# Optimization experiments

Measured on AMD Instinct MI355X. Metric: run time of the kernel, lower is better.

Reference implementation:

```python
import jax, jax.numpy as jnp
import numpy as np

N_NODES = 50000
N_EDGES = 800000
N_FEAT = 256
HIDDEN = 64
N_CLASSES = 16
T_END = 3.0  # opt['time']; rk4 takes one step over [0, 3]


def spline_conv(x, src, dst, p, W, R, b, n):
    """SplineConv, dim=1, kernel_size=2, degree=1 open B-spline, aggr='mean'.
    x: [n, Cin]; src/dst: [E]; p: [E,1] pseudo-coords in [0,1];
    W: [2, Cin, Cout]; R: [Cin, Cout]; b: [Cout]."""
    xj = x[src]  # gather source node features [E, Cin]
    # basis weights for K=2, degree=1: (1-p) on kernel 0, p on kernel 1
    msg = ((1.0 - p) * xj) @ W[0] + (p * xj) @ W[1]  # [E, Cout]
    agg = jax.ops.segment_sum(msg, dst, num_segments=n)
    deg = jax.ops.segment_sum(jnp.ones((msg.shape[0], 1), msg.dtype), dst, num_segments=n)
    return agg / jnp.maximum(deg, 1.0) + x @ R + b


def setup_inputs() -> dict:
    key = jax.random.key(0)
    ks = jax.random.split(key, 20)
    x = jax.random.normal(ks[0], (N_NODES, N_FEAT), jnp.float32)
    edge_attr = jax.random.uniform(ks[1], (N_EDGES, 1), jnp.float32)
    src = jax.random.randint(ks[2], (N_EDGES,), 0, N_NODES)
    dst = jax.random.randint(ks[3], (N_EDGES,), 0, N_NODES)

    def w(k, shape, fan_in):
        s = 1.0 / np.sqrt(fan_in)
        return jax.random.uniform(k, shape, jnp.float32, -s, s)

    # conv1: num_features -> hidden
    W1 = w(ks[4], (2, N_FEAT, HIDDEN), N_FEAT)
    R1 = w(ks[5], (N_FEAT, HIDDEN), N_FEAT)
    b1 = jnp.zeros((HIDDEN,), jnp.float32)
    # ODE func: two stacked SplineConvs hidden -> hidden
    Wa = w(ks[6], (2, HIDDEN, HIDDEN), HIDDEN)
    Ra = w(ks[7], (HIDDEN, HIDDEN), HIDDEN)
    ba = jnp.zeros((HIDDEN,), jnp.float32)
    Wb = w(ks[8], (2, HIDDEN, HIDDEN), HIDDEN)
    Rb = w(ks[9], (HIDDEN, HIDDEN), HIDDEN)
    bb = jnp.zeros((HIDDEN,), jnp.float32)
    # conv2: hidden -> num_classes
    W2 = w(ks[10], (2, HIDDEN, N_CLASSES), HIDDEN)
    R2 = w(ks[11], (HIDDEN, N_CLASSES), HIDDEN)
    b2 = jnp.zeros((N_CLASSES,), jnp.float32)

    return dict(x=x, edge_attr=edge_attr, src=src, dst=dst,
                W1=W1, R1=R1, b1=b1, Wa=Wa, Ra=Ra, ba=ba,
                Wb=Wb, Rb=Rb, bb=bb, W2=W2, R2=R2, b2=b2)


def reference(x, edge_attr, src, dst, W1, R1, b1, Wa, Ra, ba, Wb, Rb, bb, W2, R2, b2):
    n = x.shape[0]
    p = edge_attr
    h = jnp.tanh(spline_conv(x, src, dst, p, W1, R1, b1, n))
    # dropout is identity in eval mode

    def f(y):  # GCNLayer: two stacked SplineConvs, no activation
        y = spline_conv(y, src, dst, p, Wa, Ra, ba, n)
        return spline_conv(y, src, dst, p, Wb, Rb, bb, n)

    # single RK4 step from t=0 to t=T_END (torchdiffeq fixed-grid rk4 on s_span=[0,3])
    k1 = f(h)
    k2 = f(h + 0.5 * T_END * k1)
    k3 = f(h + 0.5 * T_END * k2)
    k4 = f(h + T_END * k3)
    h = h + (T_END / 6.0) * (k1 + 2.0 * k2 + 2.0 * k3 + k4)

    out = jnp.tanh(spline_conv(h, src, dst, p, W2, R2, b2, n))
    return jax.nn.log_softmax(out, axis=1)
```

## Files before the change

### kernel.cpp

```cpp
#include <hip/hip_runtime.h>
#include <math.h>

static inline int ceil_div(int a, int b) { return (a + b - 1) / b; }


__global__ __launch_bounds__(256) void zero2(int* __restrict__ a, int* __restrict__ b,
                                             int n) {
    int i = blockIdx.x * 256 + threadIdx.x;
    if (i < n) { a[i] = 0; b[i] = 0; }
}

__global__ __launch_bounds__(256) void hist_kernel(const int* __restrict__ dst,
                                                   int* __restrict__ deg, int E) {
    int e = blockIdx.x * 256 + threadIdx.x;
    if (e < E) atomicAdd(&deg[dst[e]], 1);
}

__global__ __launch_bounds__(256) void scan_blocksum(const int* __restrict__ deg,
                                                     int* __restrict__ bsum, int n) {
    __shared__ int red[256];
    int t = threadIdx.x;
    int base = blockIdx.x * 2048 + t * 8;
    int s = 0;
    #pragma unroll
    for (int i = 0; i < 8; ++i) {
        int idx = base + i;
        if (idx < n) s += deg[idx];
    }
    red[t] = s;
    __syncthreads();
    #pragma unroll
    for (int off = 128; off >= 1; off >>= 1) {
        if (t < off) red[t] += red[t + off];
        __syncthreads();
    }
    if (t == 0) bsum[blockIdx.x] = red[0];
}

__global__ __launch_bounds__(256) void scan_tops(int* __restrict__ bsum, int nb) {
    __shared__ int sh[256];
    int t = threadIdx.x;
    int orig = (t < nb) ? bsum[t] : 0;
    sh[t] = orig;
    __syncthreads();
    for (int off = 1; off < 256; off <<= 1) {
        int add = (t >= off) ? sh[t - off] : 0;
        __syncthreads();
        sh[t] += add;
        __syncthreads();
    }
    if (t < nb) bsum[t] = sh[t] - orig;
}

__global__ __launch_bounds__(256) void scan_final(const int* __restrict__ deg,
                                                  const int* __restrict__ bsum,
                                                  int* __restrict__ rowp,
                                                  float* __restrict__ invd,
                                                  int n, int E) {
    __shared__ int sh[256];
    int t = threadIdx.x;
    int base = blockIdx.x * 2048 + t * 8;
    int loc[8];
    int s = 0;
    #pragma unroll
    for (int i = 0; i < 8; ++i) {
        int idx = base + i;
        int d = (idx < n) ? deg[idx] : 0;
        loc[i] = d;
        s += d;
    }
    sh[t] = s;
    __syncthreads();
    for (int off = 1; off < 256; off <<= 1) {
        int add = (t >= off) ? sh[t - off] : 0;
        __syncthreads();
        sh[t] += add;
        __syncthreads();
    }
    int run = bsum[blockIdx.x] + (sh[t] - s);
    #pragma unroll
    for (int i = 0; i < 8; ++i) {
        int idx = base + i;
        if (idx < n) {
            rowp[idx] = run;
            int d = loc[i];
            run += d;
            invd[idx] = 1.0f / (float)(d > 1 ? d : 1);
        }
    }
    if (blockIdx.x == 0 && t == 0) rowp[n] = E;
}

__global__ __launch_bounds__(256) void scatter_idx(const int* __restrict__ dst,
                                                   const int* __restrict__ rowp,
                                                   int* __restrict__ fill,
                                                   int* __restrict__ ei, int E) {
    int e = blockIdx.x * 256 + threadIdx.x;
    if (e >= E) return;
    int d = dst[e];
    int pos = rowp[d] + atomicAdd(&fill[d], 1);
    ei[pos] = e;
}

__global__ __launch_bounds__(256) void sort_fill(const int* __restrict__ rowp,
                                                 int* __restrict__ ei,
                                                 const int* __restrict__ src,
                                                 const float* __restrict__ p,
                                                 int* __restrict__ es,
                                                 float* __restrict__ ep, int n) {
    int node = blockIdx.x * 256 + threadIdx.x;
    if (node >= n) return;
    int b = rowp[node], e = rowp[node + 1];
    for (int i = b + 1; i < e; ++i) {
        int key = ei[i];
        int j = i - 1;
        while (j >= b && ei[j] > key) { ei[j + 1] = ei[j]; --j; }
        ei[j + 1] = key;
    }
    for (int i = b; i < e; ++i) {
        int id = ei[i];
        es[i] = src[id];
        ep[i] = p[id];
    }
}

__global__ __launch_bounds__(256) void pack_all(
    const float* __restrict__ W1, const float* __restrict__ R1,
    const float* __restrict__ Wa, const float* __restrict__ Ra,
    const float* __restrict__ Wb, const float* __restrict__ Rb,
    const float* __restrict__ W2, const float* __restrict__ R2,
    float* __restrict__ Bc1, float* __restrict__ Bca,
    float* __restrict__ Bcb, float* __restrict__ Bc2) {
    int idx = blockIdx.x * 256 + threadIdx.x;
    const int S1 = 256 * 192, S2 = 192 * 64, S4 = 64 * 48;
    if (idx < S1) {
        int k = idx / 192, c = idx % 192;
        float v;
        if (c < 64)       v = W1[k * 64 + c];
        else if (c < 128) v = W1[256 * 64 + k * 64 + (c - 64)];
        else              v = R1[k * 64 + (c - 128)];
        Bc1[idx] = v;
        return;
    }
    idx -= S1;
    if (idx < S2) { Bca[idx] = (idx < 8192) ? Wa[idx] : Ra[idx - 8192]; return; }
    idx -= S2;
    if (idx < S2) { Bcb[idx] = (idx < 8192) ? Wb[idx] : Rb[idx - 8192]; return; }
    idx -= S2;
    if (idx < S4) {
        int k = idx / 48, c = idx % 48;
        float v;
        if (c < 16)      v = W2[k * 16 + c];
        else if (c < 32) v = W2[64 * 16 + k * 16 + (c - 16)];
        else             v = R2[k * 16 + (c - 32)];
        Bc2[idx] = v;
    }
}

__global__ __launch_bounds__(256) void edge_agg64_v4(const float* __restrict__ x,
                                                     const int* __restrict__ rowp,
                                                     const int* __restrict__ es,
                                                     const float* __restrict__ ep,
                                                     const float* __restrict__ invd,
                                                     float* __restrict__ agg, int n) {
    int gid = blockIdx.x * 256 + threadIdx.x;
    int node = gid >> 4;
    if (node >= n) return;
    int c4 = (gid & 15) << 2;
    int e = rowp[node], eend = rowp[node + 1];
    float sx = 0.f, sy = 0.f, sz = 0.f, sw = 0.f;
    float px = 0.f, py = 0.f, pz = 0.f, pw = 0.f;
    for (; e + 4 <= eend; e += 4) {
        int s0 = es[e], s1 = es[e + 1], s2 = es[e + 2], s3 = es[e + 3];
        float p0 = ep[e], p1 = ep[e + 1], p2 = ep[e + 2], p3 = ep[e + 3];
        float4 v0 = *reinterpret_cast<const float4*>(&x[(size_t)s0 * 64 + c4]);
        float4 v1 = *reinterpret_cast<const float4*>(&x[(size_t)s1 * 64 + c4]);
        float4 v2 = *reinterpret_cast<const float4*>(&x[(size_t)s2 * 64 + c4]);
        float4 v3 = *reinterpret_cast<const float4*>(&x[(size_t)s3 * 64 + c4]);
        sx += (v0.x + v1.x) + (v2.x + v3.x);
        sy += (v0.y + v1.y) + (v2.y + v3.y);
        sz += (v0.z + v1.z) + (v2.z + v3.z);
        sw += (v0.w + v1.w) + (v2.w + v3.w);
        px = fmaf(p0, v0.x, fmaf(p1, v1.x, fmaf(p2, v2.x, fmaf(p3, v3.x, px))));
        py = fmaf(p0, v0.y, fmaf(p1, v1.y, fmaf(p2, v2.y, fmaf(p3, v3.y, py))));
        pz = fmaf(p0, v0.z, fmaf(p1, v1.z, fmaf(p2, v2.z, fmaf(p3, v3.z, pz))));
        pw = fmaf(p0, v0.w, fmaf(p1, v1.w, fmaf(p2, v2.w, fmaf(p3, v3.w, pw))));
    }
    for (; e < eend; ++e) {
        int s = es[e];
        float pe = ep[e];
        float4 v = *reinterpret_cast<const float4*>(&x[(size_t)s * 64 + c4]);
        sx += v.x; sy += v.y; sz += v.z; sw += v.w;
        px = fmaf(pe, v.x, px); py = fmaf(pe, v.y, py);
        pz = fmaf(pe, v.z, pz); pw = fmaf(pe, v.w, pw);
    }
    float w = invd[node];
    float4 a0 = make_float4((sx - px) * w, (sy - py) * w, (sz - pz) * w, (sw - pw) * w);
    float4 a1 = make_float4(px * w, py * w, pz * w, pw * w);
    *reinterpret_cast<float4*>(&agg[(size_t)node * 128 + c4]) = a0;
    *reinterpret_cast<float4*>(&agg[(size_t)node * 128 + 64 + c4]) = a1;
}

__global__ __launch_bounds__(256) void hidden_gemm_db(
    const float* __restrict__ agg, const float* __restrict__ in,
    const float* __restrict__ B, const float* __restrict__ bias,
    int n, int mode, float* __restrict__ u_out,
    const float* __restrict__ hbuf, const float* __restrict__ acc_in,
    float* __restrict__ acc_out, float* __restrict__ t_out,
    float c1, float c2, float c3) {
    __shared__ __align__(16) float As[2][16][68];
    __shared__ __align__(16) float Bs[2][16][68];
    const int t = threadIdx.x;
    const int row0 = blockIdx.x * 64;
    const int ty = t >> 4, tx = t & 15;
    const int lrow = t >> 2, lk = (t & 3) << 2;
    const int bkk = t >> 4, bcol = (t & 15) << 2;

    float4 av = make_float4(0.f, 0.f, 0.f, 0.f);
    {
        int r = row0 + lrow;
        if (r < n) av = *reinterpret_cast<const float4*>(&agg[(size_t)r * 128 + lk]);
    }
    float4 bv = *reinterpret_cast<const float4*>(&B[(size_t)bkk * 64 + bcol]);
    As[0][lk + 0][lrow] = av.x; As[0][lk + 1][lrow] = av.y;
    As[0][lk + 2][lrow] = av.z; As[0][lk + 3][lrow] = av.w;
    *reinterpret_cast<float4*>(&Bs[0][bkk][bcol]) = bv;
    __syncthreads();

    float acc[4][4];
    #pragma unroll
    for (int i = 0; i < 4; ++i)
        #pragma unroll
        for (int j = 0; j < 4; ++j) acc[i][j] = 0.f;

    for (int kt = 0; kt < 12; ++kt) {
        const int cur = kt & 1;
        if (kt + 1 < 12) {
            int k0 = (kt + 1) << 4;
            int r = row0 + lrow;
            int kk = k0 + lk;
            av = make_float4(0.f, 0.f, 0.f, 0.f);
            if (r < n)
                av = (kk < 128)
                    ? *reinterpret_cast<const float4*>(&agg[(size_t)r * 128 + kk])
                    : *reinterpret_cast<const float4*>(&in[(size_t)r * 64 + (kk - 128)]);
            bv = *reinterpret_cast<const float4*>(&B[(size_t)(k0 + bkk) * 64 + bcol]);
        }
        #pragma unroll
        for (int kk = 0; kk < 16; ++kk) {
            float4 a4 = *reinterpret_cast<const float4*>(&As[cur][kk][ty << 2]);
            float4 b4 = *reinterpret_cast<const float4*>(&Bs[cur][kk][tx << 2]);
            float aa[4] = {a4.x, a4.y, a4.z, a4.w};
            float bb[4] = {b4.x, b4.y, b4.z, b4.w};
            #pragma unroll
            for (int i = 0; i < 4; ++i)
                #pragma unroll
                for (int j = 0; j < 4; ++j)
                    acc[i][j] = fmaf(aa[i], bb[j], acc[i][j]);
        }
        if (kt + 1 < 12) {
            const int nx = cur ^ 1;
            As[nx][lk + 0][lrow] = av.x; As[nx][lk + 1][lrow] = av.y;
            As[nx][lk + 2][lrow] = av.z; As[nx][lk + 3][lrow] = av.w;
            *reinterpret_cast<float4*>(&Bs[nx][bkk][bcol]) = bv;
        }
        __syncthreads();
    }

    float4 bia = *reinterpret_cast<const float4*>(&bias[tx << 2]);
    #pragma unroll
    for (int i = 0; i < 4; ++i) {
        int r = row0 + (ty << 2) + i;
        if (r >= n) continue;
        size_t idx = (size_t)r * 64 + (tx << 2);
        float4 v = make_float4(acc[i][0] + bia.x, acc[i][1] + bia.y,
                               acc[i][2] + bia.z, acc[i][3] + bia.w);
        if (mode == 0) {
            *reinterpret_cast<float4*>(&u_out[idx]) = v;
        } else {
            float4 ai = make_float4(0.f, 0.f, 0.f, 0.f);
            if (acc_in) ai = *reinterpret_cast<const float4*>(&acc_in[idx]);
            float4 an = make_float4(ai.x + c3 * v.x, ai.y + c3 * v.y,
                                    ai.z + c3 * v.z, ai.w + c3 * v.w);
            *reinterpret_cast<float4*>(&acc_out[idx]) = an;
            float4 hb = *reinterpret_cast<const float4*>(&hbuf[idx]);
            float4 to = make_float4(hb.x + c1 * v.x + c2 * an.x,
                                    hb.y + c1 * v.y + c2 * an.y,
                                    hb.z + c1 * v.z + c2 * an.z,
                                    hb.w + c1 * v.w + c2 * an.w);
            *reinterpret_cast<float4*>(&t_out[idx]) = to;
        }
    }
}

__global__ __launch_bounds__(128) void conv1_gemm_v3(const float* __restrict__ x,
                                                     const float* __restrict__ B,
                                                     int n, float* __restrict__ yz,
                                                     float* __restrict__ base,
                                                     const float* __restrict__ b1) {
    __shared__ __align__(16) float As[16][68];
    __shared__ __align__(16) float Bs[16][200];
    const int t = threadIdx.x;
    const int row0 = blockIdx.x * 64;
    const int ty = t >> 4, tx = t & 15;
    const int bkk0 = t >> 4, bcol = (t & 15) << 2;
    float acc[8][12];
    #pragma unroll
    for (int i = 0; i < 8; ++i)
        #pragma unroll
        for (int j = 0; j < 12; ++j) acc[i][j] = 0.f;

    for (int kt = 0; kt < 16; ++kt) {
        int k0 = kt << 4;
        #pragma unroll
        for (int hh = 0; hh < 2; ++hh) {
            int q = t + 128 * hh;
            int row = q >> 2;
            int lkq = (q & 3) << 2;
            float4 av = make_float4(0.f, 0.f, 0.f, 0.f);
            int r = row0 + row;
            if (r < n)
                av = *reinterpret_cast<const float4*>(&x[(size_t)r * 256 + k0 + lkq]);
            As[lkq + 0][row] = av.x; As[lkq + 1][row] = av.y;
            As[lkq + 2][row] = av.z; As[lkq + 3][row] = av.w;
        }
        #pragma unroll
        for (int hh = 0; hh < 2; ++hh) {
            int kk = bkk0 + 8 * hh;
            const float* bp = &B[(size_t)(k0 + kk) * 192 + bcol];
            *reinterpret_cast<float4*>(&Bs[kk][bcol])       = *reinterpret_cast<const float4*>(bp);
            *reinterpret_cast<float4*>(&Bs[kk][bcol + 64])  = *reinterpret_cast<const float4*>(bp + 64);
            *reinterpret_cast<float4*>(&Bs[kk][bcol + 128]) = *reinterpret_cast<const float4*>(bp + 128);
        }
        __syncthreads();
        #pragma unroll
        for (int kk = 0; kk < 16; ++kk) {
            float4 a0 = *reinterpret_cast<const float4*>(&As[kk][ty << 3]);
            float4 a1 = *reinterpret_cast<const float4*>(&As[kk][(ty << 3) + 4]);
            float4 b0 = *reinterpret_cast<const float4*>(&Bs[kk][tx << 2]);
            float4 b1q = *reinterpret_cast<const float4*>(&Bs[kk][(tx << 2) + 64]);
            float4 b2q = *reinterpret_cast<const float4*>(&Bs[kk][(tx << 2) + 128]);
            float aa[8] = {a0.x, a0.y, a0.z, a0.w, a1.x, a1.y, a1.z, a1.w};
            float bb[12] = {b0.x, b0.y, b0.z, b0.w, b1q.x, b1q.y, b1q.z, b1q.w,
                            b2q.x, b2q.y, b2q.z, b2q.w};
            #pragma unroll
            for (int i = 0; i < 8; ++i)
                #pragma unroll
                for (int j = 0; j < 12; ++j)
                    acc[i][j] = fmaf(aa[i], bb[j], acc[i][j]);
        }
        __syncthreads();
    }

    float4 bb4 = *reinterpret_cast<const float4*>(&b1[tx << 2]);
    #pragma unroll
    for (int i = 0; i < 8; ++i) {
        int r = row0 + (ty << 3) + i;
        if (r >= n) continue;
        float4 q0 = make_float4(acc[i][0], acc[i][1], acc[i][2], acc[i][3]);
        float4 q1 = make_float4(acc[i][4], acc[i][5], acc[i][6], acc[i][7]);
        float4 q2 = make_float4(acc[i][8] + bb4.x, acc[i][9] + bb4.y,
                                acc[i][10] + bb4.z, acc[i][11] + bb4.w);
        *reinterpret_cast<float4*>(&yz[(size_t)r * 128 + (tx << 2)]) = q0;
        *reinterpret_cast<float4*>(&yz[(size_t)r * 128 + 64 + (tx << 2)]) = q1;
        *reinterpret_cast<float4*>(&base[(size_t)r * 64 + (tx << 2)]) = q2;
    }
}

__global__ __launch_bounds__(256) void edge_tf64_v8(const float* __restrict__ yz,
                                                    const int* __restrict__ rowp,
                                                    const int* __restrict__ es,
                                                    const float* __restrict__ ep,
                                                    const float* __restrict__ invd,
                                                    const float* __restrict__ base,
                                                    float* __restrict__ out, int n) {
    int gid = blockIdx.x * 256 + threadIdx.x;
    int node = gid >> 3;
    if (node >= n) return;
    int c8 = (gid & 7) << 3;
    int e = rowp[node], eend = rowp[node + 1];
    float a[8] = {0.f, 0.f, 0.f, 0.f, 0.f, 0.f, 0.f, 0.f};
    for (; e + 2 <= eend; e += 2) {
        int s0 = es[e], s1 = es[e + 1];
        float p0 = ep[e], p1 = ep[e + 1];
        float4 y0a = *reinterpret_cast<const float4*>(&yz[(size_t)s0 * 128 + c8]);
        float4 y0b = *reinterpret_cast<const float4*>(&yz[(size_t)s0 * 128 + c8 + 4]);
        float4 z0a = *reinterpret_cast<const float4*>(&yz[(size_t)s0 * 128 + 64 + c8]);
        float4 z0b = *reinterpret_cast<const float4*>(&yz[(size_t)s0 * 128 + 64 + c8 + 4]);
        float4 y1a = *reinterpret_cast<const float4*>(&yz[(size_t)s1 * 128 + c8]);
        float4 y1b = *reinterpret_cast<const float4*>(&yz[(size_t)s1 * 128 + c8 + 4]);
        float4 z1a = *reinterpret_cast<const float4*>(&yz[(size_t)s1 * 128 + 64 + c8]);
        float4 z1b = *reinterpret_cast<const float4*>(&yz[(size_t)s1 * 128 + 64 + c8 + 4]);
        const float* ya0 = &y0a.x; const float* yb0 = &y0b.x;
        const float* za0 = &z0a.x; const float* zb0 = &z0b.x;
        const float* ya1 = &y1a.x; const float* yb1 = &y1b.x;
        const float* za1 = &z1a.x; const float* zb1 = &z1b.x;
        #pragma unroll
        for (int j = 0; j < 4; ++j) {
            a[j]     += fmaf(p0, za0[j] - ya0[j], ya0[j]) + fmaf(p1, za1[j] - ya1[j], ya1[j]);
            a[4 + j] += fmaf(p0, zb0[j] - yb0[j], yb0[j]) + fmaf(p1, zb1[j] - yb1[j], yb1[j]);
        }
    }
    for (; e < eend; ++e) {
        int s = es[e];
        float pe = ep[e];
        float4 ya = *reinterpret_cast<const float4*>(&yz[(size_t)s * 128 + c8]);
        float4 yb = *reinterpret_cast<const float4*>(&yz[(size_t)s * 128 + c8 + 4]);
        float4 za = *reinterpret_cast<const float4*>(&yz[(size_t)s * 128 + 64 + c8]);
        float4 zb = *reinterpret_cast<const float4*>(&yz[(size_t)s * 128 + 64 + c8 + 4]);
        const float* fy = &ya.x; const float* gy = &yb.x;
        const float* fz = &za.x; const float* gz = &zb.x;
        #pragma unroll
        for (int j = 0; j < 4; ++j) {
            a[j]     += fmaf(pe, fz[j] - fy[j], fy[j]);
            a[4 + j] += fmaf(pe, gz[j] - gy[j], gy[j]);
        }
    }
    float w = invd[node];
    size_t idx = (size_t)node * 64 + c8;
    float4 ba = *reinterpret_cast<const float4*>(&base[idx]);
    float4 bbv = *reinterpret_cast<const float4*>(&base[idx + 4]);
    float4 o0 = make_float4(tanhf(fmaf(a[0], w, ba.x)), tanhf(fmaf(a[1], w, ba.y)),
                            tanhf(fmaf(a[2], w, ba.z)), tanhf(fmaf(a[3], w, ba.w)));
    float4 o1 = make_float4(tanhf(fmaf(a[4], w, bbv.x)), tanhf(fmaf(a[5], w, bbv.y)),
                            tanhf(fmaf(a[6], w, bbv.z)), tanhf(fmaf(a[7], w, bbv.w)));
    *reinterpret_cast<float4*>(&out[idx]) = o0;
    *reinterpret_cast<float4*>(&out[idx + 4]) = o1;
}

__global__ __launch_bounds__(256) void edge_tf16_lsm(const float* __restrict__ yz,
                                                     const int* __restrict__ rowp,
                                                     const int* __restrict__ es,
                                                     const float* __restrict__ ep,
                                                     const float* __restrict__ invd,
                                                     const float* __restrict__ base,
                                                     float* __restrict__ out, int n) {
    int gid = blockIdx.x * 256 + threadIdx.x;
    int node = gid >> 4;
    if (node >= n) return;
    int c = gid & 15;
    int e = rowp[node], eend = rowp[node + 1];
    float a = 0.f;
    for (; e + 4 <= eend; e += 4) {
        int s0 = es[e], s1 = es[e + 1], s2 = es[e + 2], s3 = es[e + 3];
        float p0 = ep[e], p1 = ep[e + 1], p2 = ep[e + 2], p3 = ep[e + 3];
        float y0 = yz[(size_t)s0 * 32 + c],      z0 = yz[(size_t)s0 * 32 + 16 + c];
        float y1 = yz[(size_t)s1 * 32 + c],      z1 = yz[(size_t)s1 * 32 + 16 + c];
        float y2 = yz[(size_t)s2 * 32 + c],      z2 = yz[(size_t)s2 * 32 + 16 + c];
        float y3 = yz[(size_t)s3 * 32 + c],      z3 = yz[(size_t)s3 * 32 + 16 + c];
        a += fmaf(p0, z0 - y0, y0);
        a += fmaf(p1, z1 - y1, y1);
        a += fmaf(p2, z2 - y2, y2);
        a += fmaf(p3, z3 - y3, y3);
    }
    for (; e < eend; ++e) {
        int s = es[e]; float pe = ep[e];
        float y = yz[(size_t)s * 32 + c], z = yz[(size_t)s * 32 + 16 + c];
        a += fmaf(pe, z - y, y);
    }
    float o = tanhf(a * invd[node] + base[(size_t)node * 16 + c]);
    float m = o;
    #pragma unroll
    for (int off = 8; off >= 1; off >>= 1) m = fmaxf(m, __shfl_xor(m, off, 16));
    float ex = expf(o - m);
    float s = ex;
    #pragma unroll
    for (int off = 8; off >= 1; off >>= 1) s += __shfl_xor(s, off, 16);
    out[(size_t)node * 16 + c] = (o - m) - logf(s);
}

__global__ __launch_bounds__(256) void gemm_tiled(
    const float* __restrict__ A0, int lda0, int K0,
    const float* __restrict__ A1, int lda1,
    const float* __restrict__ B,
    int n, int K, int M,
    float* __restrict__ out0, int w0, const float* __restrict__ bias0,
    float* __restrict__ out1, int w1, const float* __restrict__ bias1,
    int split) {
    __shared__ __align__(16) float As[16][68];
    __shared__ __align__(16) float Bs[16][68];
    const int t = threadIdx.x;
    const int row0 = blockIdx.x * 64;
    const int col0 = blockIdx.y * 64;
    const int ty = t >> 4, tx = t & 15;
    const int lrow = t >> 2, lk = (t & 3) << 2;
    const int bkk = t >> 4, bcol = (t & 15) << 2;
    float acc[4][4];
    #pragma unroll
    for (int i = 0; i < 4; ++i)
        #pragma unroll
        for (int j = 0; j < 4; ++j) acc[i][j] = 0.f;

    for (int k0 = 0; k0 < K; k0 += 16) {
        float4 av = make_float4(0.f, 0.f, 0.f, 0.f);
        {
            int r = row0 + lrow;
            if (r < n) {
                int kk = k0 + lk;
                const float* src = (kk < K0)
                    ? (A0 + (size_t)r * lda0 + kk)
                    : (A1 + (size_t)r * lda1 + (kk - K0));
                av = *reinterpret_cast<const float4*>(src);
            }
        }
        float4 bv = make_float4(0.f, 0.f, 0.f, 0.f);
        {
            int c = col0 + bcol;
            int kk = k0 + bkk;
            if (c < M) bv = *reinterpret_cast<const float4*>(B + (size_t)kk * M + c);
        }
        As[lk + 0][lrow] = av.x; As[lk + 1][lrow] = av.y;
        As[lk + 2][lrow] = av.z; As[lk + 3][lrow] = av.w;
        *reinterpret_cast<float4*>(&Bs[bkk][bcol]) = bv;
        __syncthreads();
        #pragma unroll
        for (int kk = 0; kk < 16; ++kk) {
            float4 a4 = *reinterpret_cast<const float4*>(&As[kk][ty << 2]);
            float4 b4 = *reinterpret_cast<const float4*>(&Bs[kk][tx << 2]);
            float aa[4] = {a4.x, a4.y, a4.z, a4.w};
            float bb[4] = {b4.x, b4.y, b4.z, b4.w};
            #pragma unroll
            for (int i = 0; i < 4; ++i)
                #pragma unroll
                for (int j = 0; j < 4; ++j)
                    acc[i][j] = fmaf(aa[i], bb[j], acc[i][j]);
        }
        __syncthreads();
    }

    #pragma unroll
    for (int i = 0; i < 4; ++i) {
        int r = row0 + (ty << 2) + i;
        if (r >= n) continue;
        #pragma unroll
        for (int j = 0; j < 4; ++j) {
            int c = col0 + (tx << 2) + j;
            if (c >= M) continue;
            float v = acc[i][j];
            if (c < split) {
                if (bias0) v += bias0[c];
                out0[(size_t)r * w0 + c] = v;
            } else {
                int cc = c - split;
                if (bias1) v += bias1[cc];
                out1[(size_t)r * w1 + cc] = v;
            }
        }
    }
}


static void hidden_conv(hipStream_t stream, const float* in, float* agg,
                        const int* rowp, const int* es, const float* ep,
                        const float* invd, const float* Bc, const float* bias, int n,
                        int mode, float* u_out,
                        const float* h, const float* acc_in, float* acc_out,
                        float* t_out, float c1, float c2, float c3) {
    edge_agg64_v4<<<ceil_div(n * 16, 256), 256, 0, stream>>>(in, rowp, es, ep, invd,
                                                             agg, n);
    hidden_gemm_db<<<ceil_div(n, 64), 256, 0, stream>>>(agg, in, Bc, bias, n, mode,
                                                        u_out, h, acc_in, acc_out,
                                                        t_out, c1, c2, c3);
}

extern "C" void kernel_launch(void* const* d_in, const int* in_sizes, int n_in,
                              void* d_out, int out_size, void* d_ws, size_t ws_size,
                              hipStream_t stream) {
    const float* x  = (const float*)d_in[0];
    const float* pE = (const float*)d_in[1];
    const int*   sr = (const int*)d_in[2];
    const int*   ds = (const int*)d_in[3];
    const float* W1 = (const float*)d_in[4];
    const float* R1 = (const float*)d_in[5];
    const float* b1 = (const float*)d_in[6];
    const float* Wa = (const float*)d_in[7];
    const float* Ra = (const float*)d_in[8];
    const float* ba = (const float*)d_in[9];
    const float* Wb = (const float*)d_in[10];
    const float* Rb = (const float*)d_in[11];
    const float* bb = (const float*)d_in[12];
    const float* W2 = (const float*)d_in[13];
    const float* R2 = (const float*)d_in[14];
    const float* b2 = (const float*)d_in[15];
    const int n = in_sizes[0] / 256;
    const int E = in_sizes[2];
    float* out = (float*)d_out;

    char* w = (char*)d_ws;
    auto alloc = [&](size_t bytes) -> void* {
        void* ptr = (void*)w;
        w += (bytes + 255) & ~(size_t)255;
        return ptr;
    };
    int nscan = ceil_div(n, 2048);
    int*   deg  = (int*)alloc((size_t)n * 4);
    int*   fill = (int*)alloc((size_t)n * 4);
    int*   rowp = (int*)alloc((size_t)(n + 1) * 4);
    float* invd = (float*)alloc((size_t)n * 4);
    int*   bsum = (int*)alloc((size_t)256 * 4);
    int*   ei   = (int*)alloc((size_t)E * 4);
    int*   es   = (int*)alloc((size_t)E * 4);
    float* ep   = (float*)alloc((size_t)E * 4);
    float* Bc1  = (float*)alloc((size_t)256 * 192 * 4);
    float* Bca  = (float*)alloc((size_t)192 * 64 * 4);
    float* Bcb  = (float*)alloc((size_t)192 * 64 * 4);
    float* Bc2  = (float*)alloc((size_t)64 * 48 * 4);
    float* big0 = (float*)alloc((size_t)n * 128 * 4);
    float* big1 = (float*)alloc((size_t)n * 64 * 4);
    float* h    = (float*)alloc((size_t)n * 64 * 4);
    float* u    = (float*)alloc((size_t)n * 64 * 4);
    float* tb   = (float*)alloc((size_t)n * 64 * 4);
    float* acc  = (float*)alloc((size_t)n * 64 * 4);

    const int PACK_TOTAL = 256 * 192 + 2 * 192 * 64 + 64 * 48;

    zero2<<<ceil_div(n, 256), 256, 0, stream>>>(deg, fill, n);
    pack_all<<<ceil_div(PACK_TOTAL, 256), 256, 0, stream>>>(W1, R1, Wa, Ra, Wb, Rb,
                                                            W2, R2, Bc1, Bca, Bcb, Bc2);
    hist_kernel<<<ceil_div(E, 256), 256, 0, stream>>>(ds, deg, E);
    scan_blocksum<<<nscan, 256, 0, stream>>>(deg, bsum, n);
    scan_tops<<<1, 256, 0, stream>>>(bsum, nscan);
    scan_final<<<nscan, 256, 0, stream>>>(deg, bsum, rowp, invd, n, E);
    scatter_idx<<<ceil_div(E, 256), 256, 0, stream>>>(ds, rowp, fill, ei, E);
    sort_fill<<<ceil_div(n, 256), 256, 0, stream>>>(rowp, ei, sr, pE, es, ep, n);

    conv1_gemm_v3<<<ceil_div(n, 64), 128, 0, stream>>>(x, Bc1, n, big0, big1, b1);
    edge_tf64_v8<<<ceil_div(n * 8, 256), 256, 0, stream>>>(big0, rowp, es, ep, invd,
                                                           big1, h, n);

    hidden_conv(stream, h, big0, rowp, es, ep, invd, Bca, ba, n, 0, u,
                nullptr, nullptr, nullptr, nullptr, 0.f, 0.f, 0.f);
    hidden_conv(stream, u, big0, rowp, es, ep, invd, Bcb, bb, n, 1, nullptr,
                h, nullptr, acc, tb, 1.5f, 0.f, 1.f);
    hidden_conv(stream, tb, big0, rowp, es, ep, invd, Bca, ba, n, 0, u,
                nullptr, nullptr, nullptr, nullptr, 0.f, 0.f, 0.f);
    hidden_conv(stream, u, big0, rowp, es, ep, invd, Bcb, bb, n, 1, nullptr,
                h, acc, acc, tb, 1.5f, 0.f, 2.f);
    hidden_conv(stream, tb, big0, rowp, es, ep, invd, Bca, ba, n, 0, u,
                nullptr, nullptr, nullptr, nullptr, 0.f, 0.f, 0.f);
    hidden_conv(stream, u, big0, rowp, es, ep, invd, Bcb, bb, n, 1, nullptr,
                h, acc, acc, tb, 3.f, 0.f, 2.f);
    hidden_conv(stream, tb, big0, rowp, es, ep, invd, Bca, ba, n, 0, u,
                nullptr, nullptr, nullptr, nullptr, 0.f, 0.f, 0.f);
    hidden_conv(stream, u, big0, rowp, es, ep, invd, Bcb, bb, n, 1, nullptr,
                h, acc, acc, tb, 0.f, 0.5f, 1.f);

    gemm_tiled<<<dim3(ceil_div(n, 64), 1), 256, 0, stream>>>(
        tb, 64, 64, nullptr, 0, Bc2, n, 64, 48,
        big0, 32, nullptr, big1, 16, b2, 32);
    edge_tf16_lsm<<<ceil_div(n * 16, 256), 256, 0, stream>>>(big0, rowp, es, ep, invd,
                                                             big1, out, n);
}
```

Baseline: 878.9 us.

## Read GEMM weight tiles directly from global/cache instead of LDS, merge setup kernels

The hidden, conv1 and conv2 GEMM kernels stop staging the weight matrix B in shared memory and instead load B rows straight from global memory inside the inner loop. The small weights are expected to stay in cache, and this frees LDS and removes store/sync work. conv1 moves to 256 threads with a 4x12 per-thread tile, and conv2 gets a specialised kernel in which only 12 of 16 column threads compute. The zero and pack setup kernels are merged into one grid-stride launch. The trade-off is more global/L1 load instructions per FMA in the inner loops.

```diff
diff --git a/kernel.cpp b/kernel.cpp
--- a/kernel.cpp
+++ b/kernel.cpp
@@ -4,10 +4,42 @@
 static inline int ceil_div(int a, int b) { return (a + b - 1) / b; }
 
 
-__global__ __launch_bounds__(256) void zero2(int* __restrict__ a, int* __restrict__ b,
-                                             int n) {
-    int i = blockIdx.x * 256 + threadIdx.x;
-    if (i < n) { a[i] = 0; b[i] = 0; }
+__global__ __launch_bounds__(256) void setup_zero_pack(
+    int* __restrict__ deg, int* __restrict__ fill, int n,
+    const float* __restrict__ W1, const float* __restrict__ R1,
+    const float* __restrict__ Wa, const float* __restrict__ Ra,
+    const float* __restrict__ Wb, const float* __restrict__ Rb,
+    const float* __restrict__ W2, const float* __restrict__ R2,
+    float* __restrict__ Bc1, float* __restrict__ Bca,
+    float* __restrict__ Bcb, float* __restrict__ Bc2) {
+    int gid = blockIdx.x * 256 + threadIdx.x;
+    int gstride = gridDim.x * 256;
+    for (int i = gid; i < n; i += gstride) { deg[i] = 0; fill[i] = 0; }
+    const int S1 = 256 * 192, S2 = 192 * 64, S4 = 64 * 48;
+    const int TOT = S1 + 2 * S2 + S4;
+    for (int i0 = gid; i0 < TOT; i0 += gstride) {
+        int idx = i0;
+        if (idx < S1) {
+            int k = idx / 192, c = idx % 192;
+            float v;
+            if (c < 64)       v = W1[k * 64 + c];
+            else if (c < 128) v = W1[256 * 64 + k * 64 + (c - 64)];
+            else              v = R1[k * 64 + (c - 128)];
+            Bc1[idx] = v;
+            continue;
+        }
+        idx -= S1;
+        if (idx < S2) { Bca[idx] = (idx < 8192) ? Wa[idx] : Ra[idx - 8192]; continue; }
+        idx -= S2;
+        if (idx < S2) { Bcb[idx] = (idx < 8192) ? Wb[idx] : Rb[idx - 8192]; continue; }
+        idx -= S2;
+        int k = idx / 48, c = idx % 48;
+        float v;
+        if (c < 16)      v = W2[k * 16 + c];
+        else if (c < 32) v = W2[64 * 16 + k * 16 + (c - 16)];
+        else             v = R2[k * 16 + (c - 32)];
+        Bc2[idx] = v;
+    }
 }
 
 __global__ __launch_bounds__(256) void hist_kernel(const int* __restrict__ dst,
@@ -121,39 +153,6 @@
         int id = ei[i];
         es[i] = src[id];
         ep[i] = p[id];
-    }
-}
-
-__global__ __launch_bounds__(256) void pack_all(
-    const float* __restrict__ W1, const float* __restrict__ R1,
-    const float* __restrict__ Wa, const float* __restrict__ Ra,
-    const float* __restrict__ Wb, const float* __restrict__ Rb,
-    const float* __restrict__ W2, const float* __restrict__ R2,
-    float* __restrict__ Bc1, float* __restrict__ Bca,
-    float* __restrict__ Bcb, float* __restrict__ Bc2) {
-    int idx = blockIdx.x * 256 + threadIdx.x;
-    const int S1 = 256 * 192, S2 = 192 * 64, S4 = 64 * 48;
-    if (idx < S1) {
-        int k = idx / 192, c = idx % 192;
-        float v;
-        if (c < 64)       v = W1[k * 64 + c];
-        else if (c < 128) v = W1[256 * 64 + k * 64 + (c - 64)];
-        else              v = R1[k * 64 + (c - 128)];
-        Bc1[idx] = v;
-        return;
-    }
-    idx -= S1;
-    if (idx < S2) { Bca[idx] = (idx < 8192) ? Wa[idx] : Ra[idx - 8192]; return; }
-    idx -= S2;
-    if (idx < S2) { Bcb[idx] = (idx < 8192) ? Wb[idx] : Rb[idx - 8192]; return; }
-    idx -= S2;
-    if (idx < S4) {
-        int k = idx / 48, c = idx % 48;
-        float v;
-        if (c < 16)      v = W2[k * 16 + c];
-        else if (c < 32) v = W2[64 * 16 + k * 16 + (c - 16)];
-        else             v = R2[k * 16 + (c - 32)];
-        Bc2[idx] = v;
     }
 }
 
@@ -201,7 +200,7 @@
     *reinterpret_cast<float4*>(&agg[(size_t)node * 128 + 64 + c4]) = a1;
 }
 
-__global__ __launch_bounds__(256) void hidden_gemm_db(
+__global__ __launch_bounds__(256) void hidden_gemm_h(
     const float* __restrict__ agg, const float* __restrict__ in,
     const float* __restrict__ B, const float* __restrict__ bias,
     int n, int mode, float* __restrict__ u_out,
@@ -209,22 +208,18 @@
     float* __restrict__ acc_out, float* __restrict__ t_out,
     float c1, float c2, float c3) {
     __shared__ __align__(16) float As[2][16][68];
-    __shared__ __align__(16) float Bs[2][16][68];
     const int t = threadIdx.x;
     const int row0 = blockIdx.x * 64;
     const int ty = t >> 4, tx = t & 15;
     const int lrow = t >> 2, lk = (t & 3) << 2;
-    const int bkk = t >> 4, bcol = (t & 15) << 2;
 
     float4 av = make_float4(0.f, 0.f, 0.f, 0.f);
     {
         int r = row0 + lrow;
         if (r < n) av = *reinterpret_cast<const float4*>(&agg[(size_t)r * 128 + lk]);
     }
-    float4 bv = *reinterpret_cast<const float4*>(&B[(size_t)bkk * 64 + bcol]);
     As[0][lk + 0][lrow] = av.x; As[0][lk + 1][lrow] = av.y;
     As[0][lk + 2][lrow] = av.z; As[0][lk + 3][lrow] = av.w;
-    *reinterpret_cast<float4*>(&Bs[0][bkk][bcol]) = bv;
     __syncthreads();
 
     float acc[4][4];
@@ -244,12 +239,12 @@
                 av = (kk < 128)
                     ? *reinterpret_cast<const float4*>(&agg[(size_t)r * 128 + kk])
                     : *reinterpret_cast<const float4*>(&in[(size_t)r * 64 + (kk - 128)]);
-            bv = *reinterpret_cast<const float4*>(&B[(size_t)(k0 + bkk) * 64 + bcol]);
-        }
+        }
+        const int k0c = kt << 4;
         #pragma unroll
         for (int kk = 0; kk < 16; ++kk) {
             float4 a4 = *reinterpret_cast<const float4*>(&As[cur][kk][ty << 2]);
-            float4 b4 = *reinterpret_cast<const float4*>(&Bs[cur][kk][tx << 2]);
+            float4 b4 = *reinterpret_cast<const float4*>(&B[(size_t)(k0c + kk) * 64 + (tx << 2)]);
             float aa[4] = {a4.x, a4.y, a4.z, a4.w};
             float bb[4] = {b4.x, b4.y, b4.z, b4.w};
             #pragma unroll
@@ -262,7 +257,6 @@
             const int nx = cur ^ 1;
             As[nx][lk + 0][lrow] = av.x; As[nx][lk + 1][lrow] = av.y;
             As[nx][lk + 2][lrow] = av.z; As[nx][lk + 3][lrow] = av.w;
-            *reinterpret_cast<float4*>(&Bs[nx][bkk][bcol]) = bv;
         }
         __syncthreads();
     }
@@ -293,58 +287,42 @@
     }
 }
 
-__global__ __launch_bounds__(128) void conv1_gemm_v3(const float* __restrict__ x,
-                                                     const float* __restrict__ B,
-                                                     int n, float* __restrict__ yz,
-                                                     float* __restrict__ base,
-                                                     const float* __restrict__ b1) {
+__global__ __launch_bounds__(256) void conv1_gemm_h(const float* __restrict__ x,
+                                                    const float* __restrict__ B,
+                                                    int n, float* __restrict__ yz,
+                                                    float* __restrict__ base,
+                                                    const float* __restrict__ b1) {
     __shared__ __align__(16) float As[16][68];
-    __shared__ __align__(16) float Bs[16][200];
     const int t = threadIdx.x;
     const int row0 = blockIdx.x * 64;
     const int ty = t >> 4, tx = t & 15;
-    const int bkk0 = t >> 4, bcol = (t & 15) << 2;
-    float acc[8][12];
-    #pragma unroll
-    for (int i = 0; i < 8; ++i)
+    const int lrow = t >> 2, lk = (t & 3) << 2;
+    float acc[4][12];
+    #pragma unroll
+    for (int i = 0; i < 4; ++i)
         #pragma unroll
         for (int j = 0; j < 12; ++j) acc[i][j] = 0.f;
 
     for (int kt = 0; kt < 16; ++kt) {
         int k0 = kt << 4;
-        #pragma unroll
-        for (int hh = 0; hh < 2; ++hh) {
-            int q = t + 128 * hh;
-            int row = q >> 2;
-            int lkq = (q & 3) << 2;
-            float4 av = make_float4(0.f, 0.f, 0.f, 0.f);
-            int r = row0 + row;
-            if (r < n)
-                av = *reinterpret_cast<const float4*>(&x[(size_t)r * 256 + k0 + lkq]);
-            As[lkq + 0][row] = av.x; As[lkq + 1][row] = av.y;
-            As[lkq + 2][row] = av.z; As[lkq + 3][row] = av.w;
-        }
-        #pragma unroll
-        for (int hh = 0; hh < 2; ++hh) {
-            int kk = bkk0 + 8 * hh;
-            const float* bp = &B[(size_t)(k0 + kk) * 192 + bcol];
-            *reinterpret_cast<float4*>(&Bs[kk][bcol])       = *reinterpret_cast<const float4*>(bp);
-            *reinterpret_cast<float4*>(&Bs[kk][bcol + 64])  = *reinterpret_cast<const float4*>(bp + 64);
-            *reinterpret_cast<float4*>(&Bs[kk][bcol + 128]) = *reinterpret_cast<const float4*>(bp + 128);
-        }
+        float4 av = make_float4(0.f, 0.f, 0.f, 0.f);
+        int r = row0 + lrow;
+        if (r < n) av = *reinterpret_cast<const float4*>(&x[(size_t)r * 256 + k0 + lk]);
+        As[lk + 0][lrow] = av.x; As[lk + 1][lrow] = av.y;
+        As[lk + 2][lrow] = av.z; As[lk + 3][lrow] = av.w;
         __syncthreads();
         #pragma unroll
         for (int kk = 0; kk < 16; ++kk) {
-            float4 a0 = *reinterpret_cast<const float4*>(&As[kk][ty << 3]);
-            float4 a1 = *reinterpret_cast<const float4*>(&As[kk][(ty << 3) + 4]);
-            float4 b0 = *reinterpret_cast<const float4*>(&Bs[kk][tx << 2]);
-            float4 b1q = *reinterpret_cast<const float4*>(&Bs[kk][(tx << 2) + 64]);
-            float4 b2q = *reinterpret_cast<const float4*>(&Bs[kk][(tx << 2) + 128]);
-            float aa[8] = {a0.x, a0.y, a0.z, a0.w, a1.x, a1.y, a1.z, a1.w};
-            float bb[12] = {b0.x, b0.y, b0.z, b0.w, b1q.x, b1q.y, b1q.z, b1q.w,
-                            b2q.x, b2q.y, b2q.z, b2q.w};
+            float4 a4 = *reinterpret_cast<const float4*>(&As[kk][ty << 2]);
+            const float* bp = &B[(size_t)(k0 + kk) * 192 + (tx << 2)];
+            float4 b0 = *reinterpret_cast<const float4*>(bp);
+            float4 b1v = *reinterpret_cast<const float4*>(bp + 64);
+            float4 b2v = *reinterpret_cast<const float4*>(bp + 128);
+            float aa[4] = {a4.x, a4.y, a4.z, a4.w};
+            float bb[12] = {b0.x, b0.y, b0.z, b0.w, b1v.x, b1v.y, b1v.z, b1v.w,
+                            b2v.x, b2v.y, b2v.z, b2v.w};
             #pragma unroll
-            for (int i = 0; i < 8; ++i)
+            for (int i = 0; i < 4; ++i)
                 #pragma unroll
                 for (int j = 0; j < 12; ++j)
                     acc[i][j] = fmaf(aa[i], bb[j], acc[i][j]);
@@ -354,8 +332,8 @@
 
     float4 bb4 = *reinterpret_cast<const float4*>(&b1[tx << 2]);
     #pragma unroll
-    for (int i = 0; i < 8; ++i) {
-        int r = row0 + (ty << 3) + i;
+    for (int i = 0; i < 4; ++i) {
+        int r = row0 + (ty << 2) + i;
         if (r >= n) continue;
         float4 q0 = make_float4(acc[i][0], acc[i][1], acc[i][2], acc[i][3]);
         float4 q1 = make_float4(acc[i][4], acc[i][5], acc[i][6], acc[i][7]);
@@ -469,81 +447,60 @@
     out[(size_t)node * 16 + c] = (o - m) - logf(s);
 }
 
-__global__ __launch_bounds__(256) void gemm_tiled(
-    const float* __restrict__ A0, int lda0, int K0,
-    const float* __restrict__ A1, int lda1,
-    const float* __restrict__ B,
-    int n, int K, int M,
-    float* __restrict__ out0, int w0, const float* __restrict__ bias0,
-    float* __restrict__ out1, int w1, const float* __restrict__ bias1,
-    int split) {
+__global__ __launch_bounds__(256) void conv2_gemm_h(const float* __restrict__ A,
+                                                    const float* __restrict__ B,
+                                                    int n,
+                                                    float* __restrict__ yz2,
+                                                    float* __restrict__ base2,
+                                                    const float* __restrict__ b2) {
     __shared__ __align__(16) float As[16][68];
-    __shared__ __align__(16) float Bs[16][68];
     const int t = threadIdx.x;
     const int row0 = blockIdx.x * 64;
-    const int col0 = blockIdx.y * 64;
     const int ty = t >> 4, tx = t & 15;
     const int lrow = t >> 2, lk = (t & 3) << 2;
-    const int bkk = t >> 4, bcol = (t & 15) << 2;
     float acc[4][4];
     #pragma unroll
     for (int i = 0; i < 4; ++i)
         #pragma unroll
         for (int j = 0; j < 4; ++j) acc[i][j] = 0.f;
 
-    for (int k0 = 0; k0 < K; k0 += 16) {
+    const bool active = (tx < 12);
+    for (int kt = 0; kt < 4; ++kt) {
+        int k0 = kt << 4;
         float4 av = make_float4(0.f, 0.f, 0.f, 0.f);
-        {
-            int r = row0 + lrow;
-            if (r < n) {
-                int kk = k0 + lk;
-                const float* src = (kk < K0)
-                    ? (A0 + (size_t)r * lda0 + kk)
-                    : (A1 + (size_t)r * lda1 + (kk - K0));
-                av = *reinterpret_cast<const float4*>(src);
-            }
-        }
-        float4 bv = make_float4(0.f, 0.f, 0.f, 0.f);
-        {
-            int c = col0 + bcol;
-            int kk = k0 + bkk;
-            if (c < M) bv = *reinterpret_cast<const float4*>(B + (size_t)kk * M + c);
-        }
+        int r = row0 + lrow;
+        if (r < n) av = *reinterpret_cast<const float4*>(&A[(size_t)r * 64 + k0 + lk]);
         As[lk + 0][lrow] = av.x; As[lk + 1][lrow] = av.y;
         As[lk + 2][lrow] = av.z; As[lk + 3][lrow] = av.w;
-        *reinterpret_cast<float4*>(&Bs[bkk][bcol]) = bv;
-        __syncthreads();
-        #pragma unroll
-        for (int kk = 0; kk < 16; ++kk) {
-            float4 a4 = *reinterpret_cast<const float4*>(&As[kk][ty << 2]);
-            float4 b4 = *reinterpret_cast<const float4*>(&Bs[kk][tx << 2]);
-            float aa[4] = {a4.x, a4.y, a4.z, a4.w};
-            float bb[4] = {b4.x, b4.y, b4.z, b4.w};
+        __syncthreads();
+        if (active) {
             #pragma unroll
-            for (int i = 0; i < 4; ++i)
+            for (int kk = 0; kk < 16; ++kk) {
+                float4 a4 = *reinterpret_cast<const float4*>(&As[kk][ty << 2]);
+                float4 b4 = *reinterpret_cast<const float4*>(&B[(size_t)(k0 + kk) * 48 + (tx << 2)]);
+                float aa[4] = {a4.x, a4.y, a4.z, a4.w};
+                float bb[4] = {b4.x, b4.y, b4.z, b4.w};
                 #pragma unroll
-                for (int j = 0; j < 4; ++j)
-                    acc[i][j] = fmaf(aa[i], bb[j], acc[i][j]);
-        }
-        __syncthreads();
-    }
-
-    #pragma unroll
-    for (int i = 0; i < 4; ++i) {
-        int r = row0 + (ty << 2) + i;
-        if (r >= n) continue;
-        #pragma unroll
-        for (int j = 0; j < 4; ++j) {
-            int c = col0 + (tx << 2) + j;
-            if (c >= M) continue;
-            float v = acc[i][j];
-            if (c < split) {
-                if (bias0) v += bias0[c];
-                out0[(size_t)r * w0 + c] = v;
-            } else {
-                int cc = c - split;
-                if (bias1) v += bias1[cc];
-                out1[(size_t)r * w1 + cc] = v;
+                for (int i = 0; i < 4; ++i)
+                    #pragma unroll
+                    for (int j = 0; j < 4; ++j)
+                        acc[i][j] = fmaf(aa[i], bb[j], acc[i][j]);
+            }
+        }
+        __syncthreads();
+    }
+
+    if (active) {
+        #pragma unroll
+        for (int i = 0; i < 4; ++i) {
+            int r = row0 + (ty << 2) + i;
+            if (r >= n) continue;
+            #pragma unroll
+            for (int j = 0; j < 4; ++j) {
+                int c = (tx << 2) + j;
+                float v = acc[i][j];
+                if (c < 32) yz2[(size_t)r * 32 + c] = v;
+                else        base2[(size_t)r * 16 + (c - 32)] = v + b2[c - 32];
             }
         }
     }
@@ -558,9 +515,9 @@
                         float* t_out, float c1, float c2, float c3) {
     edge_agg64_v4<<<ceil_div(n * 16, 256), 256, 0, stream>>>(in, rowp, es, ep, invd,
                                                              agg, n);
-    hidden_gemm_db<<<ceil_div(n, 64), 256, 0, stream>>>(agg, in, Bc, bias, n, mode,
-                                                        u_out, h, acc_in, acc_out,
-                                                        t_out, c1, c2, c3);
+    hidden_gemm_h<<<ceil_div(n, 64), 256, 0, stream>>>(agg, in, Bc, bias, n, mode,
+                                                       u_out, h, acc_in, acc_out,
+                                                       t_out, c1, c2, c3);
 }
 
 extern "C" void kernel_launch(void* const* d_in, const int* in_sizes, int n_in,
@@ -612,11 +569,8 @@
     float* tb   = (float*)alloc((size_t)n * 64 * 4);
     float* acc  = (float*)alloc((size_t)n * 64 * 4);
 
-    const int PACK_TOTAL = 256 * 192 + 2 * 192 * 64 + 64 * 48;
-
-    zero2<<<ceil_div(n, 256), 256, 0, stream>>>(deg, fill, n);
-    pack_all<<<ceil_div(PACK_TOTAL, 256), 256, 0, stream>>>(W1, R1, Wa, Ra, Wb, Rb,
-                                                            W2, R2, Bc1, Bca, Bcb, Bc2);
+    setup_zero_pack<<<288, 256, 0, stream>>>(deg, fill, n, W1, R1, Wa, Ra, Wb, Rb,
+                                             W2, R2, Bc1, Bca, Bcb, Bc2);
     hist_kernel<<<ceil_div(E, 256), 256, 0, stream>>>(ds, deg, E);
     scan_blocksum<<<nscan, 256, 0, stream>>>(deg, bsum, n);
     scan_tops<<<1, 256, 0, stream>>>(bsum, nscan);
@@ -624,7 +578,7 @@
     scatter_idx<<<ceil_div(E, 256), 256, 0, stream>>>(ds, rowp, fill, ei, E);
     sort_fill<<<ceil_div(n, 256), 256, 0, stream>>>(rowp, ei, sr, pE, es, ep, n);
 
-    conv1_gemm_v3<<<ceil_div(n, 64), 128, 0, stream>>>(x, Bc1, n, big0, big1, b1);
+    conv1_gemm_h<<<ceil_div(n, 64), 256, 0, stream>>>(x, Bc1, n, big0, big1, b1);
     edge_tf64_v8<<<ceil_div(n * 8, 256), 256, 0, stream>>>(big0, rowp, es, ep, invd,
                                                            big1, h, n);
 
@@ -645,9 +599,7 @@
     hidden_conv(stream, u, big0, rowp, es, ep, invd, Bcb, bb, n, 1, nullptr,
                 h, acc, acc, tb, 0.f, 0.5f, 1.f);
 
-    gemm_tiled<<<dim3(ceil_div(n, 64), 1), 256, 0, stream>>>(
-        tb, 64, 64, nullptr, 0, Bc2, n, 64, 48,
-        big0, 32, nullptr, big1, 16, b2, 32);
+    conv2_gemm_h<<<ceil_div(n, 64), 256, 0, stream>>>(tb, Bc2, n, big0, big1, b2);
     edge_tf16_lsm<<<ceil_div(n * 16, 256), 256, 0, stream>>>(big0, rowp, es, ep, invd,
                                                              big1, out, n);
 }
```

Result: slower. 986.5 us (+12.2%).
